# Performance work log

Measured on AMD Instinct MI355X. Metric: run time of the kernel, lower is better.

Reference implementation:

```python
import jax, jax.numpy as jnp
import numpy as np

N = 50000      # num_nodes
E = 12500      # num hyperedges
NNZ = 400000   # incidence pairs
OBS = 64
LAT = 64
STEPS = 20     # (t1 - t0) / dt = 1.0 / 0.05
DT = 0.05
SQRT_DT = DT ** 0.5
SIGMA_INIT = 0.1


def setup_inputs() -> dict:
    key = jax.random.key(0)
    ks = jax.random.split(key, 12)
    w = lambda k, o, i: jax.random.normal(k, (o, i), dtype=jnp.float32) * (1.0 / np.sqrt(i))
    return {
        "x": jax.random.normal(ks[0], (N, OBS), dtype=jnp.float32),
        "enc_w1": w(ks[1], LAT, OBS),
        "enc_b1": jnp.zeros((LAT,), jnp.float32),
        "enc_w2": w(ks[2], LAT, LAT),
        "enc_b2": jnp.zeros((LAT,), jnp.float32),
        "conv_w": w(ks[3], LAT, LAT),
        "conv_b": jnp.zeros((LAT,), jnp.float32),
        "sigma": SIGMA_INIT * jnp.ones((LAT,), jnp.float32),
        "dec_w1": w(ks[4], LAT, LAT),
        "dec_b1": jnp.zeros((LAT,), jnp.float32),
        "dec_w2": w(ks[5], OBS, LAT),
        "dec_b2": jnp.zeros((OBS,), jnp.float32),
        "node_idx": jax.random.randint(ks[6], (NNZ,), 0, N),
        "edge_idx": jax.random.randint(ks[7], (NNZ,), 0, E),
        "seed": 0,
    }


def _mlp(x, w1, b1, w2, b2):
    # eqx.nn.MLP depth=1: linear -> relu -> linear, applied per node (vmapped == matmul)
    return jax.nn.relu(x @ w1.T + b1) @ w2.T + b2


def reference(x, enc_w1, enc_b1, enc_w2, enc_b2, conv_w, conv_b, sigma,
              dec_w1, dec_b1, dec_w2, dec_b2, node_idx, edge_idx, seed):
    # incidence degree normalization (HGNN-style), computed once
    ones = jnp.ones((NNZ,), jnp.float32)
    edge_deg_inv = 1.0 / jnp.maximum(jax.ops.segment_sum(ones, edge_idx, num_segments=E), 1.0)
    node_deg_inv = 1.0 / jnp.maximum(jax.ops.segment_sum(ones, node_idx, num_segments=N), 1.0)

    def conv(y):
        m = y @ conv_w.T                                                    # [N, LAT]
        e = jax.ops.segment_sum(m[node_idx], edge_idx, num_segments=E)     # node -> hyperedge
        e = e * edge_deg_inv[:, None]
        out = jax.ops.segment_sum(e[edge_idx], node_idx, num_segments=N)   # hyperedge -> node
        return out * node_deg_inv[:, None] + conv_b

    def step(y, k):
        dw = jax.random.normal(k, (N, LAT), dtype=y.dtype)
        drift = jnp.tanh(conv(y))                       # activation(conv) drift
        y = y + drift * DT + sigma * SQRT_DT * dw       # Euler-Maruyama, diagonal noise
        return y, None

    z0 = _mlp(x, enc_w1, enc_b1, enc_w2, enc_b2)        # encode (n, obs) -> (n, lat)
    keys = jax.random.split(jax.random.key(seed), STEPS)
    z1, _ = jax.lax.scan(step, z0, keys)
    return _mlp(z1, dec_w1, dec_b1, dec_w2, dec_b2)     # decode at t1
```

## Files before the change

kernel.cpp:

```cpp
#include <hip/hip_runtime.h>
#include <stdint.h>

#define N_NODES 50000
#define N_EDGES 12500
#define NNZV    400000
#define STEPS   20
#define DT_F    0.05f
#define SQRTDT_F 0.22360679774997896f

__device__ __forceinline__ float rdlf(float v, int l) {
  return __uint_as_float(__builtin_amdgcn_readlane(__float_as_uint(v), (unsigned)l));
}
__device__ __forceinline__ int rdli(int v, int l) {
  return (int)__builtin_amdgcn_readlane((unsigned)v, (unsigned)l);
}

__device__ __forceinline__ void tf2x32(uint32_t k0, uint32_t k1,
                                       uint32_t x0, uint32_t x1,
                                       uint32_t& o0, uint32_t& o1) {
  uint32_t k2 = k0 ^ k1 ^ 0x1BD11BDAu;
#define TFR(r) { x0 += x1; x1 = (x1 << (r)) | (x1 >> (32 - (r))); x1 ^= x0; }
  x0 += k0; x1 += k1;
  TFR(13) TFR(15) TFR(26) TFR(6)   x0 += k1; x1 += k2 + 1u;
  TFR(17) TFR(29) TFR(16) TFR(24)  x0 += k2; x1 += k0 + 2u;
  TFR(13) TFR(15) TFR(26) TFR(6)   x0 += k0; x1 += k1 + 3u;
  TFR(17) TFR(29) TFR(16) TFR(24)  x0 += k1; x1 += k2 + 4u;
  TFR(13) TFR(15) TFR(26) TFR(6)   x0 += k2; x1 += k0 + 5u;
#undef TFR
  o0 = x0; o1 = x1;
}

__device__ __forceinline__ float erfinv_xla(float x) {
  float w = -log1pf(-x * x);
  float p;
  if (w < 5.0f) {
    w = w - 2.5f;
    p =              2.81022636e-08f;
    p = fmaf(p, w,   3.43273939e-07f);
    p = fmaf(p, w,  -3.5233877e-06f);
    p = fmaf(p, w,  -4.39150654e-06f);
    p = fmaf(p, w,   0.00021858087f);
    p = fmaf(p, w,  -0.00125372503f);
    p = fmaf(p, w,  -0.00417768164f);
    p = fmaf(p, w,   0.246640727f);
    p = fmaf(p, w,   1.50140941f);
  } else {
    w = sqrtf(w) - 3.0f;
    p =             -0.000200214257f;
    p = fmaf(p, w,   0.000100950558f);
    p = fmaf(p, w,   0.00134934322f);
    p = fmaf(p, w,  -0.00367342844f);
    p = fmaf(p, w,   0.00573950773f);
    p = fmaf(p, w,  -0.0076224613f);
    p = fmaf(p, w,   0.00943887047f);
    p = fmaf(p, w,   1.00167406f);
    p = fmaf(p, w,   2.83297682f);
  }
  return p * x;
}

__device__ __forceinline__ float bits_to_normal(uint32_t b) {
  float f = __uint_as_float((b >> 9) | 0x3f800000u) - 1.0f;
  const float lo = -0.99999994f;
  float u = fmaf(f, 2.0f, lo);
  u = fmaxf(u, lo);
  return 1.41421356237f * erfinv_xla(u);
}

__global__ void k_keys(const int* __restrict__ seed, unsigned* __restrict__ keys) {
  int j = threadIdx.x;
  if (j < STEPS) {
    unsigned s = (unsigned)seed[0];
    unsigned o0, o1;
    tf2x32(0u, s, 0u, (unsigned)j, o0, o1);
    keys[2 * j] = o0; keys[2 * j + 1] = o1;
  }
}

__global__ void k_zero(int* __restrict__ p, int n) {
  int i = blockIdx.x * 256 + threadIdx.x;
  if (i < n) p[i] = 0;
}

__global__ void k_hist(const int* __restrict__ nidx, const int* __restrict__ eidx,
                       int* __restrict__ ecnt, int* __restrict__ ncnt) {
  int i = blockIdx.x * 256 + threadIdx.x;
  if (i < NNZV) {
    atomicAdd(&ecnt[eidx[i]], 1);
    atomicAdd(&ncnt[nidx[i]], 1);
  }
}

__global__ __launch_bounds__(256) void k_reduce(const int* __restrict__ cnt, int len,
                                                int* __restrict__ bsum) {
  __shared__ int sh[256];
  int b = blockIdx.x, tid = threadIdx.x;
  int base = b * 1024 + tid * 4;
  int s = 0;
#pragma unroll
  for (int j = 0; j < 4; ++j) {
    int i = base + j;
    if (i < len) s += cnt[i];
  }
  sh[tid] = s;
  __syncthreads();
  for (int off = 128; off > 0; off >>= 1) {
    if (tid < off) sh[tid] += sh[tid + off];
    __syncthreads();
  }
  if (tid == 0) bsum[b] = sh[0];
}

__global__ __launch_bounds__(256) void k_scanb(int* __restrict__ bsum, int nb) {
  __shared__ int sh[256];
  int tid = threadIdx.x;
  int v = (tid < nb) ? bsum[tid] : 0;
  sh[tid] = v;
  __syncthreads();
  for (int off = 1; off < 256; off <<= 1) {
    int t = (tid >= off) ? sh[tid - off] : 0;
    __syncthreads();
    sh[tid] += t;
    __syncthreads();
  }
  if (tid < nb) bsum[tid] = sh[tid] - v;
}

__global__ __launch_bounds__(256) void k_scatter(const int* __restrict__ cnt,
                                                 const int* __restrict__ bsum, int len,
                                                 int* __restrict__ start,
                                                 int* __restrict__ fill,
                                                 float* __restrict__ dinv) {
  __shared__ int sh[256];
  int b = blockIdx.x, tid = threadIdx.x;
  int base = b * 1024 + tid * 4;
  int c[4], lex[4];
  int s = 0;
#pragma unroll
  for (int j = 0; j < 4; ++j) {
    int i = base + j;
    c[j] = (i < len) ? cnt[i] : 0;
    lex[j] = s;
    s += c[j];
  }
  sh[tid] = s;
  __syncthreads();
  for (int off = 1; off < 256; off <<= 1) {
    int t = (tid >= off) ? sh[tid - off] : 0;
    __syncthreads();
    sh[tid] += t;
    __syncthreads();
  }
  int off0 = bsum[b] + sh[tid] - s;
#pragma unroll
  for (int j = 0; j < 4; ++j) {
    int i = base + j;
    if (i < len) {
      start[i] = off0 + lex[j];
      fill[i] = 0;
      dinv[i] = 1.0f / (float)(c[j] > 1 ? c[j] : 1);
    }
  }
}

__global__ void k_fill(const int* __restrict__ nidx, const int* __restrict__ eidx,
                       const int* __restrict__ estart, const int* __restrict__ nstart,
                       int* __restrict__ efill, int* __restrict__ nfill,
                       int* __restrict__ emem, int* __restrict__ nmem) {
  int i = blockIdx.x * 256 + threadIdx.x;
  if (i < NNZV) {
    int e = eidx[i], n = nidx[i];
    int pe = atomicAdd(&efill[e], 1);
    emem[estart[e] + pe] = n;
    int pn = atomicAdd(&nfill[n], 1);
    nmem[nstart[n] + pn] = e;
  }
}

__device__ __forceinline__ void stage_swz(const float* __restrict__ w,
                                          float* __restrict__ lds, int tid) {
  for (int idx = tid; idx < 4096; idx += 256) {
    int j = idx >> 6, k = idx & 63;
    lds[k * 64 + (j ^ k)] = w[idx];
  }
}

__device__ __forceinline__ float seg_gather_sum(const float* __restrict__ rows,
                                                const int* __restrict__ mem,
                                                int start, int deg, int lane) {
  float acc0 = 0.f, acc1 = 0.f;
  for (int base = 0; base < deg; base += 64) {
    int rem = min(64, deg - base);
    int ids = (lane < rem) ? mem[start + base + lane] : 0;
    int i = 0;
    for (; i + 8 <= rem; i += 8) {
      int i0 = rdli(ids, i),     i1 = rdli(ids, i + 1);
      int i2 = rdli(ids, i + 2), i3 = rdli(ids, i + 3);
      int i4 = rdli(ids, i + 4), i5 = rdli(ids, i + 5);
      int i6 = rdli(ids, i + 6), i7 = rdli(ids, i + 7);
      float v0 = rows[(size_t)i0 * 64 + lane], v1 = rows[(size_t)i1 * 64 + lane];
      float v2 = rows[(size_t)i2 * 64 + lane], v3 = rows[(size_t)i3 * 64 + lane];
      float v4 = rows[(size_t)i4 * 64 + lane], v5 = rows[(size_t)i5 * 64 + lane];
      float v6 = rows[(size_t)i6 * 64 + lane], v7 = rows[(size_t)i7 * 64 + lane];
      acc0 += (v0 + v1) + (v2 + v3);
      acc1 += (v4 + v5) + (v6 + v7);
    }
    for (; i + 4 <= rem; i += 4) {
      int i0 = rdli(ids, i),     i1 = rdli(ids, i + 1);
      int i2 = rdli(ids, i + 2), i3 = rdli(ids, i + 3);
      float v0 = rows[(size_t)i0 * 64 + lane], v1 = rows[(size_t)i1 * 64 + lane];
      float v2 = rows[(size_t)i2 * 64 + lane], v3 = rows[(size_t)i3 * 64 + lane];
      acc0 += (v0 + v1) + (v2 + v3);
    }
    for (; i < rem; ++i) acc0 += rows[(size_t)rdli(ids, i) * 64 + lane];
  }
  return acc0 + acc1;
}

__global__ __launch_bounds__(256) void k_encoder(
    const float* __restrict__ x, const float* __restrict__ w1,
    const float* __restrict__ b1, const float* __restrict__ w2,
    const float* __restrict__ b2, float* __restrict__ y) {
  __shared__ float lw1[4096], lw2[4096];
  int tid = threadIdx.x;
  stage_swz(w1, lw1, tid);
  stage_swz(w2, lw2, tid);
  __syncthreads();
  int lane = tid & 63, wave = tid >> 6;
  float w1r[64], w2r[64];
#pragma unroll
  for (int k = 0; k < 64; ++k) {
    w1r[k] = lw1[k * 64 + (lane ^ k)];
    w2r[k] = lw2[k * 64 + (lane ^ k)];
  }
  float b1v = b1[lane], b2v = b2[lane];
  int gw = blockIdx.x * 4 + wave, nw = gridDim.x * 4;
  for (int n = gw; n < N_NODES; n += nw) {
    float xv = x[(size_t)n * 64 + lane];
    float a0 = 0.f, a1 = 0.f, a2 = 0.f, a3 = 0.f;
#pragma unroll
    for (int k = 0; k < 64; k += 4) {
      a0 = fmaf(rdlf(xv, k),     w1r[k],     a0);
      a1 = fmaf(rdlf(xv, k + 1), w1r[k + 1], a1);
      a2 = fmaf(rdlf(xv, k + 2), w1r[k + 2], a2);
      a3 = fmaf(rdlf(xv, k + 3), w1r[k + 3], a3);
    }
    float h = fmaxf((a0 + a1) + (a2 + a3) + b1v, 0.f);
    a0 = a1 = a2 = a3 = 0.f;
#pragma unroll
    for (int k = 0; k < 64; k += 4) {
      a0 = fmaf(rdlf(h, k),     w2r[k],     a0);
      a1 = fmaf(rdlf(h, k + 1), w2r[k + 1], a1);
      a2 = fmaf(rdlf(h, k + 2), w2r[k + 2], a2);
      a3 = fmaf(rdlf(h, k + 3), w2r[k + 3], a3);
    }
    y[(size_t)n * 64 + lane] = (a0 + a1) + (a2 + a3) + b2v;
  }
}

__global__ __launch_bounds__(256) void k_edge(
    const float* __restrict__ y, float* __restrict__ e,
    const int* __restrict__ estart, const int* __restrict__ ecnt,
    const int* __restrict__ emem, const float* __restrict__ edinv,
    const float* __restrict__ cw) {
  __shared__ float lcw[4096];
  int tid = threadIdx.x;
  stage_swz(cw, lcw, tid);
  __syncthreads();
  int lane = tid & 63, wave = tid >> 6;
  float cwr[64];
#pragma unroll
  for (int k = 0; k < 64; ++k) cwr[k] = lcw[k * 64 + (lane ^ k)];
  int gw = blockIdx.x * 4 + wave, nw = gridDim.x * 4;
  for (int ed = gw; ed < N_EDGES; ed += nw) {
    int start = estart[ed], deg = ecnt[ed];
    float acc = seg_gather_sum(y, emem, start, deg, lane);
    float a0 = 0.f, a1 = 0.f, a2 = 0.f, a3 = 0.f;
#pragma unroll
    for (int k = 0; k < 64; k += 4) {
      a0 = fmaf(rdlf(acc, k),     cwr[k],     a0);
      a1 = fmaf(rdlf(acc, k + 1), cwr[k + 1], a1);
      a2 = fmaf(rdlf(acc, k + 2), cwr[k + 2], a2);
      a3 = fmaf(rdlf(acc, k + 3), cwr[k + 3], a3);
    }
    e[(size_t)ed * 64 + lane] = ((a0 + a1) + (a2 + a3)) * edinv[ed];
  }
}

__global__ __launch_bounds__(256) void k_node(
    const float* __restrict__ e, float* __restrict__ y,
    const int* __restrict__ nstart, const int* __restrict__ ncnt,
    const int* __restrict__ nmem, const float* __restrict__ ndinv,
    const float* __restrict__ cb, const float* __restrict__ sigma,
    const unsigned* __restrict__ keys, int s) {
  int tid = threadIdx.x;
  int lane = tid & 63, wave = tid >> 6;
  float cbv = cb[lane];
  float sgv = sigma[lane] * SQRTDT_F;
  unsigned ka = keys[2 * s], kb = keys[2 * s + 1];
  int gw = blockIdx.x * 4 + wave, nw = gridDim.x * 4;
  for (int n = gw; n < N_NODES; n += nw) {
    uint32_t r0, r1;
    tf2x32(ka, kb, 0u, (unsigned)(n * 64 + lane), r0, r1);
    float dw = bits_to_normal(r0 ^ r1);
    float acc = seg_gather_sum(e, nmem, nstart[n], ncnt[n], lane);
    float yv = y[(size_t)n * 64 + lane];
    yv = yv + tanhf(fmaf(acc, ndinv[n], cbv)) * DT_F + sgv * dw;
    y[(size_t)n * 64 + lane] = yv;
  }
}

__global__ __launch_bounds__(256) void k_decoder(
    const float* __restrict__ y, const float* __restrict__ w1,
    const float* __restrict__ b1, const float* __restrict__ w2,
    const float* __restrict__ b2, float* __restrict__ out) {
  __shared__ float lw1[4096], lw2[4096];
  int tid = threadIdx.x;
  stage_swz(w1, lw1, tid);
  stage_swz(w2, lw2, tid);
  __syncthreads();
  int lane = tid & 63, wave = tid >> 6;
  float w1r[64], w2r[64];
#pragma unroll
  for (int k = 0; k < 64; ++k) {
    w1r[k] = lw1[k * 64 + (lane ^ k)];
    w2r[k] = lw2[k * 64 + (lane ^ k)];
  }
  float b1v = b1[lane], b2v = b2[lane];
  int gw = blockIdx.x * 4 + wave, nw = gridDim.x * 4;
  for (int n = gw; n < N_NODES; n += nw) {
    float xv = y[(size_t)n * 64 + lane];
    float a0 = 0.f, a1 = 0.f, a2 = 0.f, a3 = 0.f;
#pragma unroll
    for (int k = 0; k < 64; k += 4) {
      a0 = fmaf(rdlf(xv, k),     w1r[k],     a0);
      a1 = fmaf(rdlf(xv, k + 1), w1r[k + 1], a1);
      a2 = fmaf(rdlf(xv, k + 2), w1r[k + 2], a2);
      a3 = fmaf(rdlf(xv, k + 3), w1r[k + 3], a3);
    }
    float h = fmaxf((a0 + a1) + (a2 + a3) + b1v, 0.f);
    a0 = a1 = a2 = a3 = 0.f;
#pragma unroll
    for (int k = 0; k < 64; k += 4) {
      a0 = fmaf(rdlf(h, k),     w2r[k],     a0);
      a1 = fmaf(rdlf(h, k + 1), w2r[k + 1], a1);
      a2 = fmaf(rdlf(h, k + 2), w2r[k + 2], a2);
      a3 = fmaf(rdlf(h, k + 3), w2r[k + 3], a3);
    }
    out[(size_t)n * 64 + lane] = (a0 + a1) + (a2 + a3) + b2v;
  }
}

extern "C" void kernel_launch(void* const* d_in, const int* in_sizes, int n_in,
                              void* d_out, int out_size, void* d_ws, size_t ws_size,
                              hipStream_t stream) {
  (void)in_sizes; (void)n_in; (void)out_size; (void)ws_size;
  const float* x      = (const float*)d_in[0];
  const float* enc_w1 = (const float*)d_in[1];
  const float* enc_b1 = (const float*)d_in[2];
  const float* enc_w2 = (const float*)d_in[3];
  const float* enc_b2 = (const float*)d_in[4];
  const float* conv_w = (const float*)d_in[5];
  const float* conv_b = (const float*)d_in[6];
  const float* sigma  = (const float*)d_in[7];
  const float* dec_w1 = (const float*)d_in[8];
  const float* dec_b1 = (const float*)d_in[9];
  const float* dec_w2 = (const float*)d_in[10];
  const float* dec_b2 = (const float*)d_in[11];
  const int* node_idx = (const int*)d_in[12];
  const int* edge_idx = (const int*)d_in[13];
  const int* seed     = (const int*)d_in[14];

  char* wsb = (char*)d_ws;
  size_t off = 0;
  auto alloc = [&](size_t bytes) -> void* {
    void* p = wsb + off;
    off = (off + bytes + 255) & ~(size_t)255;
    return p;
  };
  float* y        = (float*)alloc((size_t)N_NODES * 64 * 4);
  float* e        = (float*)alloc((size_t)N_EDGES * 64 * 4);
  int* edge_cnt   = (int*)alloc((size_t)N_EDGES * 4);
  int* node_cnt   = (int*)alloc((size_t)N_NODES * 4);
  int* edge_start = (int*)alloc((size_t)N_EDGES * 4);
  int* node_start = (int*)alloc((size_t)N_NODES * 4);
  int* edge_fill  = (int*)alloc((size_t)N_EDGES * 4);
  int* node_fill  = (int*)alloc((size_t)N_NODES * 4);
  int* edge_mem   = (int*)alloc((size_t)NNZV * 4);
  int* node_mem   = (int*)alloc((size_t)NNZV * 4);
  float* edinv    = (float*)alloc((size_t)N_EDGES * 4);
  float* ndinv    = (float*)alloc((size_t)N_NODES * 4);
  unsigned* keys  = (unsigned*)alloc(2 * STEPS * 4);
  int* ebsum      = (int*)alloc(256 * 4);
  int* nbsum      = (int*)alloc(256 * 4);

  const int EB = (N_EDGES + 1023) / 1024;
  const int NB = (N_NODES + 1023) / 1024;

  dim3 b256(256);
  hipLaunchKernelGGL(k_keys, dim3(1), dim3(64), 0, stream, seed, keys);
  hipLaunchKernelGGL(k_zero, dim3((N_EDGES + 255) / 256), b256, 0, stream, edge_cnt, N_EDGES);
  hipLaunchKernelGGL(k_zero, dim3((N_NODES + 255) / 256), b256, 0, stream, node_cnt, N_NODES);
  hipLaunchKernelGGL(k_hist, dim3((NNZV + 255) / 256), b256, 0, stream,
                     node_idx, edge_idx, edge_cnt, node_cnt);
  hipLaunchKernelGGL(k_reduce, dim3(EB), b256, 0, stream, edge_cnt, N_EDGES, ebsum);
  hipLaunchKernelGGL(k_reduce, dim3(NB), b256, 0, stream, node_cnt, N_NODES, nbsum);
  hipLaunchKernelGGL(k_scanb, dim3(1), b256, 0, stream, ebsum, EB);
  hipLaunchKernelGGL(k_scanb, dim3(1), b256, 0, stream, nbsum, NB);
  hipLaunchKernelGGL(k_scatter, dim3(EB), b256, 0, stream,
                     edge_cnt, ebsum, N_EDGES, edge_start, edge_fill, edinv);
  hipLaunchKernelGGL(k_scatter, dim3(NB), b256, 0, stream,
                     node_cnt, nbsum, N_NODES, node_start, node_fill, ndinv);
  hipLaunchKernelGGL(k_fill, dim3((NNZV + 255) / 256), b256, 0, stream,
                     node_idx, edge_idx, edge_start, node_start,
                     edge_fill, node_fill, edge_mem, node_mem);
  hipLaunchKernelGGL(k_encoder, dim3(1024), b256, 0, stream,
                     x, enc_w1, enc_b1, enc_w2, enc_b2, y);
  for (int s = 0; s < STEPS; ++s) {
    hipLaunchKernelGGL(k_edge, dim3(1024), b256, 0, stream,
                       y, e, edge_start, edge_cnt, edge_mem, edinv, conv_w);
    hipLaunchKernelGGL(k_node, dim3(2048), b256, 0, stream,
                       e, y, node_start, node_cnt, node_mem, ndinv,
                       conv_b, sigma, keys, s);
  }
  hipLaunchKernelGGL(k_decoder, dim3(1024), b256, 0, stream,
                     y, dec_w1, dec_b1, dec_w2, dec_b2, (float*)d_out);
}
```

Baseline: 1.210 ms.

## Build CSR via two-level bucketed binning and widen gather unroll to sixteen

Replaces the per-element global atomic CSR fill with a two-pass scheme. Entries are first binned into buckets of 16 edges or 64 nodes using packed keys, then each bucket is distributed in shared memory with LDS atomics. The aim is less global-atomic contention and more scattered writes landing in the same region. The segment gather loop is also unrolled to 16 loads with four accumulators to raise memory-level parallelism, and the gather is moved before the RNG in the node kernel so its latency overlaps the Threefry arithmetic. These add temporary buffers and extra setup launches and change the order in which members are listed within each segment, which changes floating-point summation order.

```diff
diff --git a/kernel.cpp b/kernel.cpp
--- a/kernel.cpp
+++ b/kernel.cpp
@@ -7,6 +7,11 @@
 #define STEPS   20
 #define DT_F    0.05f
 #define SQRTDT_F 0.22360679774997896f
+
+#define EB_SHIFT 4
+#define NB_SHIFT 6
+#define NBKT_E ((N_EDGES + (1 << EB_SHIFT) - 1) >> EB_SHIFT)
+#define NBKT_N ((N_NODES + (1 << NB_SHIFT) - 1) >> NB_SHIFT)
 
 __device__ __forceinline__ float rdlf(float v, int l) {
   return __uint_as_float(__builtin_amdgcn_readlane(__float_as_uint(v), (unsigned)l));
@@ -129,7 +134,6 @@
 __global__ __launch_bounds__(256) void k_scatter(const int* __restrict__ cnt,
                                                  const int* __restrict__ bsum, int len,
                                                  int* __restrict__ start,
-                                                 int* __restrict__ fill,
                                                  float* __restrict__ dinv) {
   __shared__ int sh[256];
   int b = blockIdx.x, tid = threadIdx.x;
@@ -157,23 +161,64 @@
     int i = base + j;
     if (i < len) {
       start[i] = off0 + lex[j];
-      fill[i] = 0;
       dinv[i] = 1.0f / (float)(c[j] > 1 ? c[j] : 1);
     }
   }
 }
 
-__global__ void k_fill(const int* __restrict__ nidx, const int* __restrict__ eidx,
-                       const int* __restrict__ estart, const int* __restrict__ nstart,
-                       int* __restrict__ efill, int* __restrict__ nfill,
-                       int* __restrict__ emem, int* __restrict__ nmem) {
+__global__ void k_tails(const int* __restrict__ estart, const int* __restrict__ nstart,
+                        int* __restrict__ etail, int* __restrict__ ntail) {
+  int i = blockIdx.x * 256 + threadIdx.x;
+  if (i < NBKT_E) etail[i] = estart[i << EB_SHIFT];
+  if (i < NBKT_N) ntail[i] = nstart[i << NB_SHIFT];
+}
+
+__global__ void k_binA(const int* __restrict__ nidx, const int* __restrict__ eidx,
+                       int* __restrict__ etail, int* __restrict__ ntail,
+                       unsigned* __restrict__ tmpE, unsigned* __restrict__ tmpN) {
   int i = blockIdx.x * 256 + threadIdx.x;
   if (i < NNZV) {
     int e = eidx[i], n = nidx[i];
-    int pe = atomicAdd(&efill[e], 1);
-    emem[estart[e] + pe] = n;
-    int pn = atomicAdd(&nfill[n], 1);
-    nmem[nstart[n] + pn] = e;
+    int pe = atomicAdd(&etail[e >> EB_SHIFT], 1);
+    tmpE[pe] = ((unsigned)e << 16) | (unsigned)n;
+    int pn = atomicAdd(&ntail[n >> NB_SHIFT], 1);
+    tmpN[pn] = ((unsigned)n << 14) | (unsigned)e;
+  }
+}
+
+__global__ __launch_bounds__(256) void k_binE(const unsigned* __restrict__ tmpE,
+                                              const int* __restrict__ estart,
+                                              int* __restrict__ emem) {
+  __shared__ int cnt[1 << EB_SHIFT];
+  int b = blockIdx.x, tid = threadIdx.x;
+  int e0 = b << EB_SHIFT;
+  int r0 = estart[e0];
+  int r1 = (b == NBKT_E - 1) ? NNZV : estart[(b + 1) << EB_SHIFT];
+  if (tid < (1 << EB_SHIFT)) cnt[tid] = 0;
+  __syncthreads();
+  for (int i = r0 + tid; i < r1; i += 256) {
+    unsigned p = tmpE[i];
+    int e = (int)(p >> 16), n = (int)(p & 0xFFFFu);
+    int pos = atomicAdd(&cnt[e - e0], 1);
+    emem[estart[e] + pos] = n;
+  }
+}
+
+__global__ __launch_bounds__(256) void k_binN(const unsigned* __restrict__ tmpN,
+                                              const int* __restrict__ nstart,
+                                              int* __restrict__ nmem) {
+  __shared__ int cnt[1 << NB_SHIFT];
+  int b = blockIdx.x, tid = threadIdx.x;
+  int n0 = b << NB_SHIFT;
+  int r0 = nstart[n0];
+  int r1 = (b == NBKT_N - 1) ? NNZV : nstart[(b + 1) << NB_SHIFT];
+  if (tid < (1 << NB_SHIFT)) cnt[tid] = 0;
+  __syncthreads();
+  for (int i = r0 + tid; i < r1; i += 256) {
+    unsigned p = tmpN[i];
+    int n = (int)(p >> 14), e = (int)(p & 0x3FFFu);
+    int pos = atomicAdd(&cnt[n - n0], 1);
+    nmem[nstart[n] + pos] = e;
   }
 }
 
@@ -188,33 +233,43 @@
 __device__ __forceinline__ float seg_gather_sum(const float* __restrict__ rows,
                                                 const int* __restrict__ mem,
                                                 int start, int deg, int lane) {
-  float acc0 = 0.f, acc1 = 0.f;
+  float acc0 = 0.f, acc1 = 0.f, acc2 = 0.f, acc3 = 0.f;
   for (int base = 0; base < deg; base += 64) {
     int rem = min(64, deg - base);
     int ids = (lane < rem) ? mem[start + base + lane] : 0;
     int i = 0;
-    for (; i + 8 <= rem; i += 8) {
-      int i0 = rdli(ids, i),     i1 = rdli(ids, i + 1);
-      int i2 = rdli(ids, i + 2), i3 = rdli(ids, i + 3);
-      int i4 = rdli(ids, i + 4), i5 = rdli(ids, i + 5);
-      int i6 = rdli(ids, i + 6), i7 = rdli(ids, i + 7);
-      float v0 = rows[(size_t)i0 * 64 + lane], v1 = rows[(size_t)i1 * 64 + lane];
-      float v2 = rows[(size_t)i2 * 64 + lane], v3 = rows[(size_t)i3 * 64 + lane];
-      float v4 = rows[(size_t)i4 * 64 + lane], v5 = rows[(size_t)i5 * 64 + lane];
-      float v6 = rows[(size_t)i6 * 64 + lane], v7 = rows[(size_t)i7 * 64 + lane];
+    for (; i + 16 <= rem; i += 16) {
+      int j0  = rdli(ids, i),      j1  = rdli(ids, i + 1);
+      int j2  = rdli(ids, i + 2),  j3  = rdli(ids, i + 3);
+      int j4  = rdli(ids, i + 4),  j5  = rdli(ids, i + 5);
+      int j6  = rdli(ids, i + 6),  j7  = rdli(ids, i + 7);
+      int j8  = rdli(ids, i + 8),  j9  = rdli(ids, i + 9);
+      int j10 = rdli(ids, i + 10), j11 = rdli(ids, i + 11);
+      int j12 = rdli(ids, i + 12), j13 = rdli(ids, i + 13);
+      int j14 = rdli(ids, i + 14), j15 = rdli(ids, i + 15);
+      float v0  = rows[(size_t)j0  * 64 + lane], v1  = rows[(size_t)j1  * 64 + lane];
+      float v2  = rows[(size_t)j2  * 64 + lane], v3  = rows[(size_t)j3  * 64 + lane];
+      float v4  = rows[(size_t)j4  * 64 + lane], v5  = rows[(size_t)j5  * 64 + lane];
+      float v6  = rows[(size_t)j6  * 64 + lane], v7  = rows[(size_t)j7  * 64 + lane];
+      float v8  = rows[(size_t)j8  * 64 + lane], v9  = rows[(size_t)j9  * 64 + lane];
+      float v10 = rows[(size_t)j10 * 64 + lane], v11 = rows[(size_t)j11 * 64 + lane];
+      float v12 = rows[(size_t)j12 * 64 + lane], v13 = rows[(size_t)j13 * 64 + lane];
+      float v14 = rows[(size_t)j14 * 64 + lane], v15 = rows[(size_t)j15 * 64 + lane];
       acc0 += (v0 + v1) + (v2 + v3);
       acc1 += (v4 + v5) + (v6 + v7);
+      acc2 += (v8 + v9) + (v10 + v11);
+      acc3 += (v12 + v13) + (v14 + v15);
     }
     for (; i + 4 <= rem; i += 4) {
-      int i0 = rdli(ids, i),     i1 = rdli(ids, i + 1);
-      int i2 = rdli(ids, i + 2), i3 = rdli(ids, i + 3);
-      float v0 = rows[(size_t)i0 * 64 + lane], v1 = rows[(size_t)i1 * 64 + lane];
-      float v2 = rows[(size_t)i2 * 64 + lane], v3 = rows[(size_t)i3 * 64 + lane];
+      int j0 = rdli(ids, i),     j1 = rdli(ids, i + 1);
+      int j2 = rdli(ids, i + 2), j3 = rdli(ids, i + 3);
+      float v0 = rows[(size_t)j0 * 64 + lane], v1 = rows[(size_t)j1 * 64 + lane];
+      float v2 = rows[(size_t)j2 * 64 + lane], v3 = rows[(size_t)j3 * 64 + lane];
       acc0 += (v0 + v1) + (v2 + v3);
     }
     for (; i < rem; ++i) acc0 += rows[(size_t)rdli(ids, i) * 64 + lane];
   }
-  return acc0 + acc1;
+  return (acc0 + acc1) + (acc2 + acc3);
 }
 
 __global__ __launch_bounds__(256) void k_encoder(
@@ -300,10 +355,10 @@
   unsigned ka = keys[2 * s], kb = keys[2 * s + 1];
   int gw = blockIdx.x * 4 + wave, nw = gridDim.x * 4;
   for (int n = gw; n < N_NODES; n += nw) {
+    float acc = seg_gather_sum(e, nmem, nstart[n], ncnt[n], lane);
     uint32_t r0, r1;
     tf2x32(ka, kb, 0u, (unsigned)(n * 64 + lane), r0, r1);
     float dw = bits_to_normal(r0 ^ r1);
-    float acc = seg_gather_sum(e, nmem, nstart[n], ncnt[n], lane);
     float yv = y[(size_t)n * 64 + lane];
     yv = yv + tanhf(fmaf(acc, ndinv[n], cbv)) * DT_F + sgv * dw;
     y[(size_t)n * 64 + lane] = yv;
@@ -384,18 +439,21 @@
   int* node_cnt   = (int*)alloc((size_t)N_NODES * 4);
   int* edge_start = (int*)alloc((size_t)N_EDGES * 4);
   int* node_start = (int*)alloc((size_t)N_NODES * 4);
-  int* edge_fill  = (int*)alloc((size_t)N_EDGES * 4);
-  int* node_fill  = (int*)alloc((size_t)N_NODES * 4);
   int* edge_mem   = (int*)alloc((size_t)NNZV * 4);
   int* node_mem   = (int*)alloc((size_t)NNZV * 4);
+  unsigned* tmpE  = (unsigned*)alloc((size_t)NNZV * 4);
+  unsigned* tmpN  = (unsigned*)alloc((size_t)NNZV * 4);
   float* edinv    = (float*)alloc((size_t)N_EDGES * 4);
   float* ndinv    = (float*)alloc((size_t)N_NODES * 4);
   unsigned* keys  = (unsigned*)alloc(2 * STEPS * 4);
   int* ebsum      = (int*)alloc(256 * 4);
   int* nbsum      = (int*)alloc(256 * 4);
+  int* etail      = (int*)alloc((size_t)NBKT_E * 4);
+  int* ntail      = (int*)alloc((size_t)NBKT_N * 4);
 
   const int EB = (N_EDGES + 1023) / 1024;
   const int NB = (N_NODES + 1023) / 1024;
+  const int TB = (NBKT_N + 255) / 256;
 
   dim3 b256(256);
   hipLaunchKernelGGL(k_keys, dim3(1), dim3(64), 0, stream, seed, keys);
@@ -408,12 +466,15 @@
   hipLaunchKernelGGL(k_scanb, dim3(1), b256, 0, stream, ebsum, EB);
   hipLaunchKernelGGL(k_scanb, dim3(1), b256, 0, stream, nbsum, NB);
   hipLaunchKernelGGL(k_scatter, dim3(EB), b256, 0, stream,
-                     edge_cnt, ebsum, N_EDGES, edge_start, edge_fill, edinv);
+                     edge_cnt, ebsum, N_EDGES, edge_start, edinv);
   hipLaunchKernelGGL(k_scatter, dim3(NB), b256, 0, stream,
-                     node_cnt, nbsum, N_NODES, node_start, node_fill, ndinv);
-  hipLaunchKernelGGL(k_fill, dim3((NNZV + 255) / 256), b256, 0, stream,
-                     node_idx, edge_idx, edge_start, node_start,
-                     edge_fill, node_fill, edge_mem, node_mem);
+                     node_cnt, nbsum, N_NODES, node_start, ndinv);
+  hipLaunchKernelGGL(k_tails, dim3(TB), b256, 0, stream,
+                     edge_start, node_start, etail, ntail);
+  hipLaunchKernelGGL(k_binA, dim3((NNZV + 255) / 256), b256, 0, stream,
+                     node_idx, edge_idx, etail, ntail, tmpE, tmpN);
+  hipLaunchKernelGGL(k_binE, dim3(NBKT_E), b256, 0, stream, tmpE, edge_start, edge_mem);
+  hipLaunchKernelGGL(k_binN, dim3(NBKT_N), b256, 0, stream, tmpN, node_start, node_mem);
   hipLaunchKernelGGL(k_encoder, dim3(1024), b256, 0, stream,
                      x, enc_w1, enc_b1, enc_w2, enc_b2, y);
   for (int s = 0; s < STEPS; ++s) {
```

After: 1.669 ms. 1.38x slower.

## Use 16-bit incidence indices and process two segments per wave with interleaved gathers

Applied to the files above, without the earlier changes.

Stores the CSR incidence member lists as unsigned short instead of int, halving index traffic. Each wave now handles two edges or two nodes at once, interleaving their row gathers to raise memory-level parallelism. The edge kernel reads conv weights from LDS instead of caching them in registers, which lowers register pressure, and grid sizes change to match. Clamped 8-wide gathers add redundant loads on short segments.

```diff
diff --git a/kernel.cpp b/kernel.cpp
--- a/kernel.cpp
+++ b/kernel.cpp
@@ -166,14 +166,14 @@
 __global__ void k_fill(const int* __restrict__ nidx, const int* __restrict__ eidx,
                        const int* __restrict__ estart, const int* __restrict__ nstart,
                        int* __restrict__ efill, int* __restrict__ nfill,
-                       int* __restrict__ emem, int* __restrict__ nmem) {
+                       unsigned short* __restrict__ emem, unsigned short* __restrict__ nmem) {
   int i = blockIdx.x * 256 + threadIdx.x;
   if (i < NNZV) {
     int e = eidx[i], n = nidx[i];
     int pe = atomicAdd(&efill[e], 1);
-    emem[estart[e] + pe] = n;
+    emem[estart[e] + pe] = (unsigned short)n;
     int pn = atomicAdd(&nfill[n], 1);
-    nmem[nstart[n] + pn] = e;
+    nmem[nstart[n] + pn] = (unsigned short)e;
   }
 }
 
@@ -185,36 +185,56 @@
   }
 }
 
-__device__ __forceinline__ float seg_gather_sum(const float* __restrict__ rows,
-                                                const int* __restrict__ mem,
-                                                int start, int deg, int lane) {
-  float acc0 = 0.f, acc1 = 0.f;
-  for (int base = 0; base < deg; base += 64) {
-    int rem = min(64, deg - base);
-    int ids = (lane < rem) ? mem[start + base + lane] : 0;
-    int i = 0;
-    for (; i + 8 <= rem; i += 8) {
-      int i0 = rdli(ids, i),     i1 = rdli(ids, i + 1);
-      int i2 = rdli(ids, i + 2), i3 = rdli(ids, i + 3);
-      int i4 = rdli(ids, i + 4), i5 = rdli(ids, i + 5);
-      int i6 = rdli(ids, i + 6), i7 = rdli(ids, i + 7);
-      float v0 = rows[(size_t)i0 * 64 + lane], v1 = rows[(size_t)i1 * 64 + lane];
-      float v2 = rows[(size_t)i2 * 64 + lane], v3 = rows[(size_t)i3 * 64 + lane];
-      float v4 = rows[(size_t)i4 * 64 + lane], v5 = rows[(size_t)i5 * 64 + lane];
-      float v6 = rows[(size_t)i6 * 64 + lane], v7 = rows[(size_t)i7 * 64 + lane];
-      acc0 += (v0 + v1) + (v2 + v3);
-      acc1 += (v4 + v5) + (v6 + v7);
-    }
-    for (; i + 4 <= rem; i += 4) {
-      int i0 = rdli(ids, i),     i1 = rdli(ids, i + 1);
-      int i2 = rdli(ids, i + 2), i3 = rdli(ids, i + 3);
-      float v0 = rows[(size_t)i0 * 64 + lane], v1 = rows[(size_t)i1 * 64 + lane];
-      float v2 = rows[(size_t)i2 * 64 + lane], v3 = rows[(size_t)i3 * 64 + lane];
-      acc0 += (v0 + v1) + (v2 + v3);
-    }
-    for (; i < rem; ++i) acc0 += rows[(size_t)rdli(ids, i) * 64 + lane];
-  }
-  return acc0 + acc1;
+__device__ __forceinline__ void seg2(const float* __restrict__ rows,
+                                     const unsigned short* __restrict__ mem,
+                                     int st0, int d0, int st1, int d1, int lane,
+                                     float& out0, float& out1) {
+  float A0 = 0.f, A1 = 0.f;
+  int b0 = 0, b1 = 0;
+  while (b0 < d0 || b1 < d1) {
+    int r0 = d0 - b0; r0 = r0 > 64 ? 64 : r0;
+    int r1 = d1 - b1; r1 = r1 > 64 ? 64 : r1;
+    int id0 = (r0 > 0 && lane < r0) ? (int)mem[st0 + b0 + lane] : 0;
+    int id1 = (r1 > 0 && lane < r1) ? (int)mem[st1 + b1 + lane] : 0;
+    int i0 = 0, i1 = 0;
+    while (i0 < r0 || i1 < r1) {
+      float v0[8], v1[8];
+      int m0 = r0 - i0;
+      int m1 = r1 - i1;
+      if (m0 > 0) {
+        int cap = r0 - 1;
+#pragma unroll
+        for (int k = 0; k < 8; ++k) {
+          int idx = i0 + k; idx = idx > cap ? cap : idx;
+          v0[k] = rows[(size_t)rdli(id0, idx) * 64 + lane];
+        }
+      }
+      if (m1 > 0) {
+        int cap = r1 - 1;
+#pragma unroll
+        for (int k = 0; k < 8; ++k) {
+          int idx = i1 + k; idx = idx > cap ? cap : idx;
+          v1[k] = rows[(size_t)rdli(id1, idx) * 64 + lane];
+        }
+      }
+      if (m0 > 0) {
+        float s = 0.f;
+#pragma unroll
+        for (int k = 0; k < 8; ++k) s += (k < m0) ? v0[k] : 0.f;
+        A0 += s;
+        i0 += 8;
+      }
+      if (m1 > 0) {
+        float s = 0.f;
+#pragma unroll
+        for (int k = 0; k < 8; ++k) s += (k < m1) ? v1[k] : 0.f;
+        A1 += s;
+        i1 += 8;
+      }
+    }
+    b0 += 64; b1 += 64;
+  }
+  out0 = A0; out1 = A1;
 }
 
 __global__ __launch_bounds__(256) void k_encoder(
@@ -261,36 +281,38 @@
 __global__ __launch_bounds__(256) void k_edge(
     const float* __restrict__ y, float* __restrict__ e,
     const int* __restrict__ estart, const int* __restrict__ ecnt,
-    const int* __restrict__ emem, const float* __restrict__ edinv,
+    const unsigned short* __restrict__ emem, const float* __restrict__ edinv,
     const float* __restrict__ cw) {
   __shared__ float lcw[4096];
   int tid = threadIdx.x;
   stage_swz(cw, lcw, tid);
   __syncthreads();
   int lane = tid & 63, wave = tid >> 6;
-  float cwr[64];
-#pragma unroll
-  for (int k = 0; k < 64; ++k) cwr[k] = lcw[k * 64 + (lane ^ k)];
+  const int NP = N_EDGES / 2;
   int gw = blockIdx.x * 4 + wave, nw = gridDim.x * 4;
-  for (int ed = gw; ed < N_EDGES; ed += nw) {
-    int start = estart[ed], deg = ecnt[ed];
-    float acc = seg_gather_sum(y, emem, start, deg, lane);
-    float a0 = 0.f, a1 = 0.f, a2 = 0.f, a3 = 0.f;
-#pragma unroll
-    for (int k = 0; k < 64; k += 4) {
-      a0 = fmaf(rdlf(acc, k),     cwr[k],     a0);
-      a1 = fmaf(rdlf(acc, k + 1), cwr[k + 1], a1);
-      a2 = fmaf(rdlf(acc, k + 2), cwr[k + 2], a2);
-      a3 = fmaf(rdlf(acc, k + 3), cwr[k + 3], a3);
-    }
-    e[(size_t)ed * 64 + lane] = ((a0 + a1) + (a2 + a3)) * edinv[ed];
+  for (int p = gw; p < NP; p += nw) {
+    int e0 = p, e1 = p + NP;
+    float s0, s1;
+    seg2(y, emem, estart[e0], ecnt[e0], estart[e1], ecnt[e1], lane, s0, s1);
+    float a00 = 0.f, a01 = 0.f, a10 = 0.f, a11 = 0.f;
+#pragma unroll
+    for (int k = 0; k < 64; k += 2) {
+      float w0 = lcw[k * 64 + (lane ^ k)];
+      float w1 = lcw[(k + 1) * 64 + (lane ^ (k + 1))];
+      a00 = fmaf(rdlf(s0, k),     w0, a00);
+      a10 = fmaf(rdlf(s1, k),     w0, a10);
+      a01 = fmaf(rdlf(s0, k + 1), w1, a01);
+      a11 = fmaf(rdlf(s1, k + 1), w1, a11);
+    }
+    e[(size_t)e0 * 64 + lane] = (a00 + a01) * edinv[e0];
+    e[(size_t)e1 * 64 + lane] = (a10 + a11) * edinv[e1];
   }
 }
 
 __global__ __launch_bounds__(256) void k_node(
     const float* __restrict__ e, float* __restrict__ y,
     const int* __restrict__ nstart, const int* __restrict__ ncnt,
-    const int* __restrict__ nmem, const float* __restrict__ ndinv,
+    const unsigned short* __restrict__ nmem, const float* __restrict__ ndinv,
     const float* __restrict__ cb, const float* __restrict__ sigma,
     const unsigned* __restrict__ keys, int s) {
   int tid = threadIdx.x;
@@ -298,15 +320,22 @@
   float cbv = cb[lane];
   float sgv = sigma[lane] * SQRTDT_F;
   unsigned ka = keys[2 * s], kb = keys[2 * s + 1];
+  const int NP = N_NODES / 2;
   int gw = blockIdx.x * 4 + wave, nw = gridDim.x * 4;
-  for (int n = gw; n < N_NODES; n += nw) {
-    uint32_t r0, r1;
-    tf2x32(ka, kb, 0u, (unsigned)(n * 64 + lane), r0, r1);
-    float dw = bits_to_normal(r0 ^ r1);
-    float acc = seg_gather_sum(e, nmem, nstart[n], ncnt[n], lane);
-    float yv = y[(size_t)n * 64 + lane];
-    yv = yv + tanhf(fmaf(acc, ndinv[n], cbv)) * DT_F + sgv * dw;
-    y[(size_t)n * 64 + lane] = yv;
+  for (int p = gw; p < NP; p += nw) {
+    int n0 = p, n1 = p + NP;
+    float s0, s1;
+    seg2(e, nmem, nstart[n0], ncnt[n0], nstart[n1], ncnt[n1], lane, s0, s1);
+    uint32_t a0, a1, c0, c1;
+    tf2x32(ka, kb, 0u, (unsigned)(n0 * 64 + lane), a0, a1);
+    tf2x32(ka, kb, 0u, (unsigned)(n1 * 64 + lane), c0, c1);
+    float dw0 = bits_to_normal(a0 ^ a1);
+    float dw1 = bits_to_normal(c0 ^ c1);
+    float y0 = y[(size_t)n0 * 64 + lane], y1 = y[(size_t)n1 * 64 + lane];
+    y0 = y0 + tanhf(fmaf(s0, ndinv[n0], cbv)) * DT_F + sgv * dw0;
+    y1 = y1 + tanhf(fmaf(s1, ndinv[n1], cbv)) * DT_F + sgv * dw1;
+    y[(size_t)n0 * 64 + lane] = y0;
+    y[(size_t)n1 * 64 + lane] = y1;
   }
 }
 
@@ -386,8 +415,8 @@
   int* node_start = (int*)alloc((size_t)N_NODES * 4);
   int* edge_fill  = (int*)alloc((size_t)N_EDGES * 4);
   int* node_fill  = (int*)alloc((size_t)N_NODES * 4);
-  int* edge_mem   = (int*)alloc((size_t)NNZV * 4);
-  int* node_mem   = (int*)alloc((size_t)NNZV * 4);
+  unsigned short* edge_mem = (unsigned short*)alloc((size_t)NNZV * 2);
+  unsigned short* node_mem = (unsigned short*)alloc((size_t)NNZV * 2);
   float* edinv    = (float*)alloc((size_t)N_EDGES * 4);
   float* ndinv    = (float*)alloc((size_t)N_NODES * 4);
   unsigned* keys  = (unsigned*)alloc(2 * STEPS * 4);
@@ -417,9 +446,9 @@
   hipLaunchKernelGGL(k_encoder, dim3(1024), b256, 0, stream,
                      x, enc_w1, enc_b1, enc_w2, enc_b2, y);
   for (int s = 0; s < STEPS; ++s) {
-    hipLaunchKernelGGL(k_edge, dim3(1024), b256, 0, stream,
+    hipLaunchKernelGGL(k_edge, dim3(1563), b256, 0, stream,
                        y, e, edge_start, edge_cnt, edge_mem, edinv, conv_w);
-    hipLaunchKernelGGL(k_node, dim3(2048), b256, 0, stream,
+    hipLaunchKernelGGL(k_node, dim3(6250), b256, 0, stream,
                        e, y, node_start, node_cnt, node_mem, ndinv,
                        conv_b, sigma, keys, s);
   }
```

Result: slower. 1.316 ms (+8.8%).

## Store gathered node/edge features in fp16 and incidence indices as uint16

Applied to the files above, without the earlier changes.

Keeps an fp16 shadow copy of the latent state and stores the hyperedge features in fp16, so both gather phases read half-width rows. Incidence member lists are also packed as 16-bit indices, and the gather loop is unrolled to 16 outstanding loads. The aim is to halve bandwidth in the memory-bound gather steps, at the cost of an extra fp16 write per node step and reduced precision in the drift. Node indices reach 50000, which fits in 16 bits unsigned. The fp16 rounding error could accumulate over the twenty steps.

```diff
diff --git a/kernel.cpp b/kernel.cpp
--- a/kernel.cpp
+++ b/kernel.cpp
@@ -1,4 +1,5 @@
 #include <hip/hip_runtime.h>
+#include <hip/hip_fp16.h>
 #include <stdint.h>
 
 #define N_NODES 50000
@@ -166,14 +167,14 @@
 __global__ void k_fill(const int* __restrict__ nidx, const int* __restrict__ eidx,
                        const int* __restrict__ estart, const int* __restrict__ nstart,
                        int* __restrict__ efill, int* __restrict__ nfill,
-                       int* __restrict__ emem, int* __restrict__ nmem) {
+                       unsigned short* __restrict__ emem, unsigned short* __restrict__ nmem) {
   int i = blockIdx.x * 256 + threadIdx.x;
   if (i < NNZV) {
     int e = eidx[i], n = nidx[i];
     int pe = atomicAdd(&efill[e], 1);
-    emem[estart[e] + pe] = n;
+    emem[estart[e] + pe] = (unsigned short)n;
     int pn = atomicAdd(&nfill[n], 1);
-    nmem[nstart[n] + pn] = e;
+    nmem[nstart[n] + pn] = (unsigned short)e;
   }
 }
 
@@ -185,42 +186,53 @@
   }
 }
 
-__device__ __forceinline__ float seg_gather_sum(const float* __restrict__ rows,
-                                                const int* __restrict__ mem,
-                                                int start, int deg, int lane) {
-  float acc0 = 0.f, acc1 = 0.f;
+__device__ __forceinline__ float seg_gather_sum_h(const __half* __restrict__ rows,
+                                                  const unsigned short* __restrict__ mem,
+                                                  int start, int deg, int lane) {
+  float acc0 = 0.f, acc1 = 0.f, acc2 = 0.f, acc3 = 0.f;
   for (int base = 0; base < deg; base += 64) {
     int rem = min(64, deg - base);
-    int ids = (lane < rem) ? mem[start + base + lane] : 0;
+    int ids = (lane < rem) ? (int)mem[start + base + lane] : 0;
     int i = 0;
-    for (; i + 8 <= rem; i += 8) {
-      int i0 = rdli(ids, i),     i1 = rdli(ids, i + 1);
-      int i2 = rdli(ids, i + 2), i3 = rdli(ids, i + 3);
-      int i4 = rdli(ids, i + 4), i5 = rdli(ids, i + 5);
-      int i6 = rdli(ids, i + 6), i7 = rdli(ids, i + 7);
-      float v0 = rows[(size_t)i0 * 64 + lane], v1 = rows[(size_t)i1 * 64 + lane];
-      float v2 = rows[(size_t)i2 * 64 + lane], v3 = rows[(size_t)i3 * 64 + lane];
-      float v4 = rows[(size_t)i4 * 64 + lane], v5 = rows[(size_t)i5 * 64 + lane];
-      float v6 = rows[(size_t)i6 * 64 + lane], v7 = rows[(size_t)i7 * 64 + lane];
-      acc0 += (v0 + v1) + (v2 + v3);
-      acc1 += (v4 + v5) + (v6 + v7);
+    for (; i + 16 <= rem; i += 16) {
+      int j0  = rdli(ids, i),      j1  = rdli(ids, i + 1);
+      int j2  = rdli(ids, i + 2),  j3  = rdli(ids, i + 3);
+      int j4  = rdli(ids, i + 4),  j5  = rdli(ids, i + 5);
+      int j6  = rdli(ids, i + 6),  j7  = rdli(ids, i + 7);
+      int j8  = rdli(ids, i + 8),  j9  = rdli(ids, i + 9);
+      int j10 = rdli(ids, i + 10), j11 = rdli(ids, i + 11);
+      int j12 = rdli(ids, i + 12), j13 = rdli(ids, i + 13);
+      int j14 = rdli(ids, i + 14), j15 = rdli(ids, i + 15);
+      __half h0  = rows[(size_t)j0  * 64 + lane], h1  = rows[(size_t)j1  * 64 + lane];
+      __half h2  = rows[(size_t)j2  * 64 + lane], h3  = rows[(size_t)j3  * 64 + lane];
+      __half h4  = rows[(size_t)j4  * 64 + lane], h5  = rows[(size_t)j5  * 64 + lane];
+      __half h6  = rows[(size_t)j6  * 64 + lane], h7  = rows[(size_t)j7  * 64 + lane];
+      __half h8  = rows[(size_t)j8  * 64 + lane], h9  = rows[(size_t)j9  * 64 + lane];
+      __half h10 = rows[(size_t)j10 * 64 + lane], h11 = rows[(size_t)j11 * 64 + lane];
+      __half h12 = rows[(size_t)j12 * 64 + lane], h13 = rows[(size_t)j13 * 64 + lane];
+      __half h14 = rows[(size_t)j14 * 64 + lane], h15 = rows[(size_t)j15 * 64 + lane];
+      acc0 += (__half2float(h0) + __half2float(h1)) + (__half2float(h2) + __half2float(h3));
+      acc1 += (__half2float(h4) + __half2float(h5)) + (__half2float(h6) + __half2float(h7));
+      acc2 += (__half2float(h8) + __half2float(h9)) + (__half2float(h10) + __half2float(h11));
+      acc3 += (__half2float(h12) + __half2float(h13)) + (__half2float(h14) + __half2float(h15));
     }
     for (; i + 4 <= rem; i += 4) {
-      int i0 = rdli(ids, i),     i1 = rdli(ids, i + 1);
-      int i2 = rdli(ids, i + 2), i3 = rdli(ids, i + 3);
-      float v0 = rows[(size_t)i0 * 64 + lane], v1 = rows[(size_t)i1 * 64 + lane];
-      float v2 = rows[(size_t)i2 * 64 + lane], v3 = rows[(size_t)i3 * 64 + lane];
-      acc0 += (v0 + v1) + (v2 + v3);
-    }
-    for (; i < rem; ++i) acc0 += rows[(size_t)rdli(ids, i) * 64 + lane];
-  }
-  return acc0 + acc1;
+      int j0 = rdli(ids, i),     j1 = rdli(ids, i + 1);
+      int j2 = rdli(ids, i + 2), j3 = rdli(ids, i + 3);
+      __half h0 = rows[(size_t)j0 * 64 + lane], h1 = rows[(size_t)j1 * 64 + lane];
+      __half h2 = rows[(size_t)j2 * 64 + lane], h3 = rows[(size_t)j3 * 64 + lane];
+      acc0 += (__half2float(h0) + __half2float(h1)) + (__half2float(h2) + __half2float(h3));
+    }
+    for (; i < rem; ++i)
+      acc0 += __half2float(rows[(size_t)rdli(ids, i) * 64 + lane]);
+  }
+  return (acc0 + acc1) + (acc2 + acc3);
 }
 
 __global__ __launch_bounds__(256) void k_encoder(
     const float* __restrict__ x, const float* __restrict__ w1,
     const float* __restrict__ b1, const float* __restrict__ w2,
-    const float* __restrict__ b2, float* __restrict__ y) {
+    const float* __restrict__ b2, float* __restrict__ y, __half* __restrict__ yh) {
   __shared__ float lw1[4096], lw2[4096];
   int tid = threadIdx.x;
   stage_swz(w1, lw1, tid);
@@ -254,14 +266,16 @@
       a2 = fmaf(rdlf(h, k + 2), w2r[k + 2], a2);
       a3 = fmaf(rdlf(h, k + 3), w2r[k + 3], a3);
     }
-    y[(size_t)n * 64 + lane] = (a0 + a1) + (a2 + a3) + b2v;
+    float z = (a0 + a1) + (a2 + a3) + b2v;
+    y[(size_t)n * 64 + lane] = z;
+    yh[(size_t)n * 64 + lane] = __float2half(z);
   }
 }
 
 __global__ __launch_bounds__(256) void k_edge(
-    const float* __restrict__ y, float* __restrict__ e,
+    const __half* __restrict__ yh, __half* __restrict__ eh,
     const int* __restrict__ estart, const int* __restrict__ ecnt,
-    const int* __restrict__ emem, const float* __restrict__ edinv,
+    const unsigned short* __restrict__ emem, const float* __restrict__ edinv,
     const float* __restrict__ cw) {
   __shared__ float lcw[4096];
   int tid = threadIdx.x;
@@ -273,8 +287,7 @@
   for (int k = 0; k < 64; ++k) cwr[k] = lcw[k * 64 + (lane ^ k)];
   int gw = blockIdx.x * 4 + wave, nw = gridDim.x * 4;
   for (int ed = gw; ed < N_EDGES; ed += nw) {
-    int start = estart[ed], deg = ecnt[ed];
-    float acc = seg_gather_sum(y, emem, start, deg, lane);
+    float acc = seg_gather_sum_h(yh, emem, estart[ed], ecnt[ed], lane);
     float a0 = 0.f, a1 = 0.f, a2 = 0.f, a3 = 0.f;
 #pragma unroll
     for (int k = 0; k < 64; k += 4) {
@@ -283,14 +296,14 @@
       a2 = fmaf(rdlf(acc, k + 2), cwr[k + 2], a2);
       a3 = fmaf(rdlf(acc, k + 3), cwr[k + 3], a3);
     }
-    e[(size_t)ed * 64 + lane] = ((a0 + a1) + (a2 + a3)) * edinv[ed];
+    eh[(size_t)ed * 64 + lane] = __float2half(((a0 + a1) + (a2 + a3)) * edinv[ed]);
   }
 }
 
 __global__ __launch_bounds__(256) void k_node(
-    const float* __restrict__ e, float* __restrict__ y,
+    const __half* __restrict__ eh, float* __restrict__ y, __half* __restrict__ yh,
     const int* __restrict__ nstart, const int* __restrict__ ncnt,
-    const int* __restrict__ nmem, const float* __restrict__ ndinv,
+    const unsigned short* __restrict__ nmem, const float* __restrict__ ndinv,
     const float* __restrict__ cb, const float* __restrict__ sigma,
     const unsigned* __restrict__ keys, int s) {
   int tid = threadIdx.x;
@@ -300,13 +313,14 @@
   unsigned ka = keys[2 * s], kb = keys[2 * s + 1];
   int gw = blockIdx.x * 4 + wave, nw = gridDim.x * 4;
   for (int n = gw; n < N_NODES; n += nw) {
+    float acc = seg_gather_sum_h(eh, nmem, nstart[n], ncnt[n], lane);
     uint32_t r0, r1;
     tf2x32(ka, kb, 0u, (unsigned)(n * 64 + lane), r0, r1);
     float dw = bits_to_normal(r0 ^ r1);
-    float acc = seg_gather_sum(e, nmem, nstart[n], ncnt[n], lane);
     float yv = y[(size_t)n * 64 + lane];
     yv = yv + tanhf(fmaf(acc, ndinv[n], cbv)) * DT_F + sgv * dw;
     y[(size_t)n * 64 + lane] = yv;
+    yh[(size_t)n * 64 + lane] = __float2half(yv);
   }
 }
 
@@ -379,15 +393,16 @@
     return p;
   };
   float* y        = (float*)alloc((size_t)N_NODES * 64 * 4);
-  float* e        = (float*)alloc((size_t)N_EDGES * 64 * 4);
+  __half* yh      = (__half*)alloc((size_t)N_NODES * 64 * 2);
+  __half* eh      = (__half*)alloc((size_t)N_EDGES * 64 * 2);
   int* edge_cnt   = (int*)alloc((size_t)N_EDGES * 4);
   int* node_cnt   = (int*)alloc((size_t)N_NODES * 4);
   int* edge_start = (int*)alloc((size_t)N_EDGES * 4);
   int* node_start = (int*)alloc((size_t)N_NODES * 4);
   int* edge_fill  = (int*)alloc((size_t)N_EDGES * 4);
   int* node_fill  = (int*)alloc((size_t)N_NODES * 4);
-  int* edge_mem   = (int*)alloc((size_t)NNZV * 4);
-  int* node_mem   = (int*)alloc((size_t)NNZV * 4);
+  unsigned short* edge_mem = (unsigned short*)alloc((size_t)NNZV * 2);
+  unsigned short* node_mem = (unsigned short*)alloc((size_t)NNZV * 2);
   float* edinv    = (float*)alloc((size_t)N_EDGES * 4);
   float* ndinv    = (float*)alloc((size_t)N_NODES * 4);
   unsigned* keys  = (unsigned*)alloc(2 * STEPS * 4);
@@ -415,12 +430,12 @@
                      node_idx, edge_idx, edge_start, node_start,
                      edge_fill, node_fill, edge_mem, node_mem);
   hipLaunchKernelGGL(k_encoder, dim3(1024), b256, 0, stream,
-                     x, enc_w1, enc_b1, enc_w2, enc_b2, y);
+                     x, enc_w1, enc_b1, enc_w2, enc_b2, y, yh);
   for (int s = 0; s < STEPS; ++s) {
     hipLaunchKernelGGL(k_edge, dim3(1024), b256, 0, stream,
-                       y, e, edge_start, edge_cnt, edge_mem, edinv, conv_w);
+                       yh, eh, edge_start, edge_cnt, edge_mem, edinv, conv_w);
     hipLaunchKernelGGL(k_node, dim3(2048), b256, 0, stream,
-                       e, y, node_start, node_cnt, node_mem, ndinv,
+                       eh, y, yh, node_start, node_cnt, node_mem, ndinv,
                        conv_b, sigma, keys, s);
   }
   hipLaunchKernelGGL(k_decoder, dim3(1024), b256, 0, stream,
```

After: 1.330 ms. 9.9% more time.
